# Kernel tuning notes

Measured on AMD Instinct MI355X. Metric: run time of the kernel, lower is better.

Reference implementation:

```python
import jax, jax.numpy as jnp
import numpy as np

B, S, D = 4, 4096, 1024


def setup_inputs() -> dict:
    key = jax.random.key(0)
    ks = jax.random.split(key, 4)
    scale = 1.0 / np.sqrt(D)
    x = jax.random.normal(ks[0], (B, S, D), dtype=jnp.float32)
    Wg = jax.random.normal(ks[1], (D, D), dtype=jnp.float32) * scale
    Wv = jax.random.normal(ks[2], (D, D), dtype=jnp.float32) * scale
    Wd = jax.random.normal(ks[3], (D, D), dtype=jnp.float32) * scale
    bg = jnp.zeros((D,), dtype=jnp.float32)
    bv = jnp.zeros((D,), dtype=jnp.float32)
    bd = jnp.ones((D,), dtype=jnp.float32)  # decay_bias_init = 1.0
    return {"x": x, "Wg": Wg, "bg": bg, "Wv": Wv, "bv": bv, "Wd": Wd, "bd": bd}


def _scan_causal(x_scan, a):
    # h_t = a_t * h_{t-1} + x_t, scanned over time; x_scan, a: [B,S,D]
    def step(h, inp):
        a_t, x_t = inp
        h = a_t * h + x_t
        return h, h

    h0 = jnp.zeros(x_scan.shape[::2], dtype=x_scan.dtype)  # [B,D]
    xs = (jnp.swapaxes(a, 0, 1), jnp.swapaxes(x_scan, 0, 1))  # [S,B,D]
    _, out = jax.lax.scan(step, h0, xs)
    return jnp.swapaxes(out, 0, 1)  # back to [B,S,D]


def reference(x, Wg, bg, Wv, bv, Wd, bd):
    # nn.Linear: y = x @ W.T + b
    g = jnp.einsum('bsd,ed->bse', x, Wg) + bg
    v = jnp.einsum('bsd,ed->bse', x, Wv) + bv
    d = jnp.einsum('bsd,ed->bse', x, Wd) + bd
    x_scan = jax.nn.sigmoid(g) * jnp.tanh(v)
    a = 0.001 + 0.998 * jax.nn.sigmoid(d)
    return _scan_causal(x_scan, a)
```

## Files before the change

### kernel.cpp

```cpp
#include <hip/hip_runtime.h>
#include <cstddef>
#include <cstdint>


typedef _Float16 f16;
typedef f16 f16x8 __attribute__((ext_vector_type(8)));
typedef float f32x4 __attribute__((ext_vector_type(4)));

#define S_LEN 4096
#define D_DIM 1024
#define B_DIM 4
#define M_TOT (B_DIM * S_LEN)
#define N_TOT (3 * D_DIM)
#define K_TOT D_DIM

#define CLEN 16
#define CPB (S_LEN / CLEN)
#define NCHUNK (B_DIM * CPB)

__device__ __forceinline__ void cvt8(const float* s, f16* d) {
  f32x4 a = *(const f32x4*)s;
  f32x4 b = *(const f32x4*)(s + 4);
  f16x8 o;
  o[0] = (f16)a[0]; o[1] = (f16)a[1]; o[2] = (f16)a[2]; o[3] = (f16)a[3];
  o[4] = (f16)b[0]; o[5] = (f16)b[1]; o[6] = (f16)b[2]; o[7] = (f16)b[3];
  *(f16x8*)d = o;
}

__global__ void cvt_all_kernel(const float* __restrict__ x, const float* __restrict__ w0,
                               const float* __restrict__ w1, const float* __restrict__ w2,
                               f16* __restrict__ Ah, f16* __restrict__ Bh) {
  int i = (blockIdx.x * 256 + threadIdx.x) * 8;
  if (i < M_TOT * K_TOT) {
    cvt8(x + i, Ah + i);
  } else {
    int w = i - M_TOT * K_TOT;
    int sel = w >> 20;
    int loc = w & 1048575;
    const float* s = (sel == 0) ? w0 : (sel == 1) ? w1 : w2;
    cvt8(s + loc, Bh + w);
  }
}

#define BM 128
#define BN 128
#define BK 32
#define CT_PITCH 136

__device__ __forceinline__ void gl_lds16(const void* g, void* l) {
  __builtin_amdgcn_global_load_lds((const __attribute__((address_space(1))) void*)g,
                                   (__attribute__((address_space(3))) void*)l, 16, 0, 0);
}

__global__ __launch_bounds__(256) void gemm_f16_kernel(const f16* __restrict__ A,
                                                       const f16* __restrict__ Bt,
                                                       f16* __restrict__ C) {
  __shared__ __attribute__((aligned(16))) char smem[BM * CT_PITCH * 2];
  f16* As = (f16*)smem;
  f16* Bs = As + 4096;
  const int tid = threadIdx.x;
  const int lane = tid & 63;
  const int wave = tid >> 6;
  const int m0 = blockIdx.y * BM;
  const int n0 = blockIdx.x * BN;

  const int srow = tid >> 2;
  const int scol = (tid & 3) * 8;
  const f16* aG0 = A + (size_t)(m0 + srow) * K_TOT + scol;
  const f16* aG1 = A + (size_t)(m0 + srow + 64) * K_TOT + scol;
  const f16* bG0 = Bt + (size_t)(n0 + srow) * K_TOT + scol;
  const f16* bG1 = Bt + (size_t)(n0 + srow + 64) * K_TOT + scol;
  f16* aL0 = As + tid * 8;
  f16* aL1 = As + 2048 + tid * 8;
  f16* bL0 = Bs + tid * 8;
  f16* bL1 = Bs + 2048 + tid * 8;

  const int wm = (wave >> 1) * 64;
  const int wn = (wave & 1) * 64;
  const int lm = lane & 15;
  const int kq = (lane >> 4) * 8;

  f32x4 acc[4][4] = {};

  for (int k0 = 0; k0 < K_TOT; k0 += BK) {
    gl_lds16(aG0 + k0, aL0);
    gl_lds16(aG1 + k0, aL1);
    gl_lds16(bG0 + k0, bL0);
    gl_lds16(bG1 + k0, bL1);
    __syncthreads();
    f16x8 af[4], bf[4];
#pragma unroll
    for (int i = 0; i < 4; ++i)
      af[i] = *(const f16x8*)&As[(wm + i * 16 + lm) * BK + kq];
#pragma unroll
    for (int j = 0; j < 4; ++j)
      bf[j] = *(const f16x8*)&Bs[(wn + j * 16 + lm) * BK + kq];
#pragma unroll
    for (int i = 0; i < 4; ++i)
#pragma unroll
      for (int j = 0; j < 4; ++j)
        acc[i][j] = __builtin_amdgcn_mfma_f32_16x16x32_f16(af[i], bf[j], acc[i][j], 0, 0, 0);
    __syncthreads();
  }

  f16* Ct = (f16*)smem;
  const int r0 = wm + (lane >> 4) * 4;
  const int c0 = wn + (lane & 15);
#pragma unroll
  for (int i = 0; i < 4; ++i)
#pragma unroll
    for (int j = 0; j < 4; ++j)
#pragma unroll
      for (int r = 0; r < 4; ++r)
        Ct[(r0 + i * 16 + r) * CT_PITCH + c0 + j * 16] = (f16)acc[i][j][r];
  __syncthreads();
#pragma unroll
  for (int p = 0; p < 8; ++p) {
    int row = p * 16 + (tid >> 4);
    int col = (tid & 15) * 8;
    *(f16x8*)(C + (size_t)(m0 + row) * N_TOT + n0 + col) =
        *(const f16x8*)&Ct[row * CT_PITCH + col];
  }
}

__global__ void scan1_kernel(const f16* __restrict__ G, const float* __restrict__ bg,
                             const float* __restrict__ bv, const float* __restrict__ bd,
                             f16* __restrict__ xsA, f16* __restrict__ aA,
                             float* __restrict__ P, float* __restrict__ H) {
  const int u = blockIdx.x * 256 + threadIdx.x;
  const int cg = u & 127;
  const int b = (u >> 7) & 3;
  const int ck = u >> 9;
  const int ch = cg * 8;
  float vbg[8], vbv[8], vbd[8];
  *(f32x4*)vbg = *(const f32x4*)(bg + ch); *(f32x4*)(vbg + 4) = *(const f32x4*)(bg + ch + 4);
  *(f32x4*)vbv = *(const f32x4*)(bv + ch); *(f32x4*)(vbv + 4) = *(const f32x4*)(bv + ch + 4);
  *(f32x4*)vbd = *(const f32x4*)(bd + ch); *(f32x4*)(vbd + 4) = *(const f32x4*)(bd + ch + 4);
  float h[8] = {}, p[8] = {1.f, 1.f, 1.f, 1.f, 1.f, 1.f, 1.f, 1.f};
  const int t0 = ck * CLEN;
#pragma unroll 2
  for (int t = t0; t < t0 + CLEN; ++t) {
    const size_t m = (size_t)b * S_LEN + t;
    const f16* gp = G + m * N_TOT + ch;
    f16x8 g8 = *(const f16x8*)gp;
    f16x8 v8 = *(const f16x8*)(gp + D_DIM);
    f16x8 d8 = *(const f16x8*)(gp + 2 * D_DIM);
    f16x8 xs8, a8;
#pragma unroll
    for (int j = 0; j < 8; ++j) {
      float gg = (float)g8[j] + vbg[j];
      float vv = (float)v8[j] + vbv[j];
      float dd = (float)d8[j] + vbd[j];
      float sg = 1.f / (1.f + __expf(-gg));
      float tv = 1.f - 2.f / (__expf(2.f * vv) + 1.f);
      float sd = 1.f / (1.f + __expf(-dd));
      f16 xh = (f16)(sg * tv);
      f16 ah = (f16)(0.001f + 0.998f * sd);
      float xsr = (float)xh, avr = (float)ah;
      h[j] = avr * h[j] + xsr;
      p[j] *= avr;
      xs8[j] = xh;
      a8[j] = ah;
    }
    *(f16x8*)(xsA + m * D_DIM + ch) = xs8;
    *(f16x8*)(aA + m * D_DIM + ch) = a8;
  }
  const int base = (b * CPB + ck) * D_DIM + ch;
  *(f32x4*)(P + base) = *(f32x4*)p;
  *(f32x4*)(P + base + 4) = *(f32x4*)(p + 4);
  *(f32x4*)(H + base) = *(f32x4*)h;
  *(f32x4*)(H + base + 4) = *(f32x4*)(h + 4);
}

__global__ void scan2_kernel(const float* __restrict__ P, const float* __restrict__ H,
                             float* __restrict__ carry) {
  const int idx = blockIdx.x * 256 + threadIdx.x;
  const int b = idx >> 10;
  const int d = idx & 1023;
  float h = 0.f;
  for (int c = 0; c < CPB; ++c) {
    int gs = b * CPB + c;
    carry[gs * D_DIM + d] = h;
    h = P[gs * D_DIM + d] * h + H[gs * D_DIM + d];
  }
}

__global__ void scan3_kernel(const f16* __restrict__ xsA, const f16* __restrict__ aA,
                             const float* __restrict__ carry, float* __restrict__ out) {
  const int u = blockIdx.x * 256 + threadIdx.x;
  const int cg = u & 127;
  const int b = (u >> 7) & 3;
  const int ck = u >> 9;
  const int ch = cg * 8;
  const int base = (b * CPB + ck) * D_DIM + ch;
  float h[8];
  *(f32x4*)h = *(const f32x4*)(carry + base);
  *(f32x4*)(h + 4) = *(const f32x4*)(carry + base + 4);
  const int t0 = ck * CLEN;
#pragma unroll 2
  for (int t = t0; t < t0 + CLEN; ++t) {
    const size_t m = (size_t)b * S_LEN + t;
    f16x8 xs8 = *(const f16x8*)(xsA + m * D_DIM + ch);
    f16x8 a8 = *(const f16x8*)(aA + m * D_DIM + ch);
#pragma unroll
    for (int j = 0; j < 8; ++j) h[j] = (float)a8[j] * h[j] + (float)xs8[j];
    float* op = out + m * D_DIM + ch;
    *(f32x4*)op = *(f32x4*)h;
    *(f32x4*)(op + 4) = *(f32x4*)(h + 4);
  }
}

extern "C" void kernel_launch(void* const* d_in, const int* in_sizes, int n_in,
                              void* d_out, int out_size, void* d_ws, size_t ws_size,
                              hipStream_t stream) {
  const float* x = (const float*)d_in[0];
  const float* Wg = (const float*)d_in[1];
  const float* bg = (const float*)d_in[2];
  const float* Wv = (const float*)d_in[3];
  const float* bv = (const float*)d_in[4];
  const float* Wd = (const float*)d_in[5];
  const float* bd = (const float*)d_in[6];
  float* out = (float*)d_out;

  char* ws = (char*)d_ws;
  f16* Ah = (f16*)(ws);
  float* P = (float*)(ws);
  float* H = (float*)(ws + 4194304);
  float* carry = (float*)(ws + 8388608);
  f16* Bh = (f16*)(ws + 33554432);
  f16* Gh = (f16*)(ws + 39845888);
  f16* xsA = (f16*)(ws + 140509184);
  f16* aA = (f16*)(ws + 174063616);

  cvt_all_kernel<<<9728, 256, 0, stream>>>(x, Wg, Wv, Wd, Ah, Bh);
  gemm_f16_kernel<<<dim3(N_TOT / BN, M_TOT / BM), 256, 0, stream>>>(Ah, Bh, Gh);
  scan1_kernel<<<512, 256, 0, stream>>>(Gh, bg, bv, bd, xsA, aA, P, H);
  scan2_kernel<<<16, 256, 0, stream>>>(P, H, carry);
  scan3_kernel<<<512, 256, 0, stream>>>(xsA, aA, carry, out);
}
```

Before: 338.2 us.

## Double GEMM K-tile to 64 and halve scan chunk length with transposed carries

The GEMM loads a 64-wide K slab per iteration as two 32-wide halves, which halves the number of barrier-separated iterations. The chunked scan uses 8-step chunks instead of 16, doubling thread count in the elementwise passes. It also stores per-chunk products and partial states transposed so the sequential carry pass can use vector loads. The trade-off is that the serial carry pass now has twice as many steps on very few threads.

```diff
diff --git a/kernel.cpp b/kernel.cpp
--- a/kernel.cpp
+++ b/kernel.cpp
@@ -14,7 +14,7 @@
 #define N_TOT (3 * D_DIM)
 #define K_TOT D_DIM
 
-#define CLEN 16
+#define CLEN 8
 #define CPB (S_LEN / CLEN)
 #define NCHUNK (B_DIM * CPB)
 
@@ -44,7 +44,6 @@
 
 #define BM 128
 #define BN 128
-#define BK 32
 #define CT_PITCH 136
 
 __device__ __forceinline__ void gl_lds16(const void* g, void* l) {
@@ -57,7 +56,7 @@
                                                        f16* __restrict__ C) {
   __shared__ __attribute__((aligned(16))) char smem[BM * CT_PITCH * 2];
   f16* As = (f16*)smem;
-  f16* Bs = As + 4096;
+  f16* Bs = As + 8192;
   const int tid = threadIdx.x;
   const int lane = tid & 63;
   const int wave = tid >> 6;
@@ -72,8 +71,12 @@
   const f16* bG1 = Bt + (size_t)(n0 + srow + 64) * K_TOT + scol;
   f16* aL0 = As + tid * 8;
   f16* aL1 = As + 2048 + tid * 8;
+  f16* aL2 = As + 4096 + tid * 8;
+  f16* aL3 = As + 6144 + tid * 8;
   f16* bL0 = Bs + tid * 8;
   f16* bL1 = Bs + 2048 + tid * 8;
+  f16* bL2 = Bs + 4096 + tid * 8;
+  f16* bL3 = Bs + 6144 + tid * 8;
 
   const int wm = (wave >> 1) * 64;
   const int wn = (wave & 1) * 64;
@@ -82,24 +85,33 @@
 
   f32x4 acc[4][4] = {};
 
-  for (int k0 = 0; k0 < K_TOT; k0 += BK) {
+  for (int k0 = 0; k0 < K_TOT; k0 += 64) {
     gl_lds16(aG0 + k0, aL0);
     gl_lds16(aG1 + k0, aL1);
+    gl_lds16(aG0 + k0 + 32, aL2);
+    gl_lds16(aG1 + k0 + 32, aL3);
     gl_lds16(bG0 + k0, bL0);
     gl_lds16(bG1 + k0, bL1);
+    gl_lds16(bG0 + k0 + 32, bL2);
+    gl_lds16(bG1 + k0 + 32, bL3);
     __syncthreads();
-    f16x8 af[4], bf[4];
-#pragma unroll
-    for (int i = 0; i < 4; ++i)
-      af[i] = *(const f16x8*)&As[(wm + i * 16 + lm) * BK + kq];
-#pragma unroll
-    for (int j = 0; j < 4; ++j)
-      bf[j] = *(const f16x8*)&Bs[(wn + j * 16 + lm) * BK + kq];
-#pragma unroll
-    for (int i = 0; i < 4; ++i)
+#pragma unroll
+    for (int h = 0; h < 2; ++h) {
+      const f16* as = As + h * 4096;
+      const f16* bs = Bs + h * 4096;
+      f16x8 af[4], bf[4];
+#pragma unroll
+      for (int i = 0; i < 4; ++i)
+        af[i] = *(const f16x8*)&as[(wm + i * 16 + lm) * 32 + kq];
 #pragma unroll
       for (int j = 0; j < 4; ++j)
-        acc[i][j] = __builtin_amdgcn_mfma_f32_16x16x32_f16(af[i], bf[j], acc[i][j], 0, 0, 0);
+        bf[j] = *(const f16x8*)&bs[(wn + j * 16 + lm) * 32 + kq];
+#pragma unroll
+      for (int i = 0; i < 4; ++i)
+#pragma unroll
+        for (int j = 0; j < 4; ++j)
+          acc[i][j] = __builtin_amdgcn_mfma_f32_16x16x32_f16(af[i], bf[j], acc[i][j], 0, 0, 0);
+    }
     __syncthreads();
   }
 
@@ -138,7 +150,7 @@
   *(f32x4*)vbd = *(const f32x4*)(bd + ch); *(f32x4*)(vbd + 4) = *(const f32x4*)(bd + ch + 4);
   float h[8] = {}, p[8] = {1.f, 1.f, 1.f, 1.f, 1.f, 1.f, 1.f, 1.f};
   const int t0 = ck * CLEN;
-#pragma unroll 2
+#pragma unroll
   for (int t = t0; t < t0 + CLEN; ++t) {
     const size_t m = (size_t)b * S_LEN + t;
     const f16* gp = G + m * N_TOT + ch;
@@ -165,23 +177,30 @@
     *(f16x8*)(xsA + m * D_DIM + ch) = xs8;
     *(f16x8*)(aA + m * D_DIM + ch) = a8;
   }
-  const int base = (b * CPB + ck) * D_DIM + ch;
-  *(f32x4*)(P + base) = *(f32x4*)p;
-  *(f32x4*)(P + base + 4) = *(f32x4*)(p + 4);
-  *(f32x4*)(H + base) = *(f32x4*)h;
-  *(f32x4*)(H + base + 4) = *(f32x4*)(h + 4);
+#pragma unroll
+  for (int j = 0; j < 8; ++j) {
+    const size_t tbase = (size_t)(b * D_DIM + ch + j) * CPB + ck;
+    P[tbase] = p[j];
+    H[tbase] = h[j];
+  }
 }
 
 __global__ void scan2_kernel(const float* __restrict__ P, const float* __restrict__ H,
                              float* __restrict__ carry) {
-  const int idx = blockIdx.x * 256 + threadIdx.x;
-  const int b = idx >> 10;
-  const int d = idx & 1023;
+  const int bd = blockIdx.x * 256 + threadIdx.x;
+  const int b = bd >> 10;
+  const int d = bd & 1023;
+  const float* Pp = P + (size_t)bd * CPB;
+  const float* Hp = H + (size_t)bd * CPB;
   float h = 0.f;
-  for (int c = 0; c < CPB; ++c) {
-    int gs = b * CPB + c;
-    carry[gs * D_DIM + d] = h;
-    h = P[gs * D_DIM + d] * h + H[gs * D_DIM + d];
+  for (int c = 0; c < CPB; c += 4) {
+    f32x4 p4 = *(const f32x4*)(Pp + c);
+    f32x4 h4 = *(const f32x4*)(Hp + c);
+    float* cp = carry + (size_t)(b * CPB + c) * D_DIM + d;
+    cp[0] = h;          h = p4[0] * h + h4[0];
+    cp[D_DIM] = h;      h = p4[1] * h + h4[1];
+    cp[2 * D_DIM] = h;  h = p4[2] * h + h4[2];
+    cp[3 * D_DIM] = h;  h = p4[3] * h + h4[3];
   }
 }
 
@@ -192,12 +211,12 @@
   const int b = (u >> 7) & 3;
   const int ck = u >> 9;
   const int ch = cg * 8;
-  const int base = (b * CPB + ck) * D_DIM + ch;
+  const size_t base = (size_t)(b * CPB + ck) * D_DIM + ch;
   float h[8];
   *(f32x4*)h = *(const f32x4*)(carry + base);
   *(f32x4*)(h + 4) = *(const f32x4*)(carry + base + 4);
   const int t0 = ck * CLEN;
-#pragma unroll 2
+#pragma unroll
   for (int t = t0; t < t0 + CLEN; ++t) {
     const size_t m = (size_t)b * S_LEN + t;
     f16x8 xs8 = *(const f16x8*)(xsA + m * D_DIM + ch);
@@ -225,8 +244,8 @@
   char* ws = (char*)d_ws;
   f16* Ah = (f16*)(ws);
   float* P = (float*)(ws);
-  float* H = (float*)(ws + 4194304);
-  float* carry = (float*)(ws + 8388608);
+  float* H = (float*)(ws + 8388608);
+  float* carry = (float*)(ws + 16777216);
   f16* Bh = (f16*)(ws + 33554432);
   f16* Gh = (f16*)(ws + 39845888);
   f16* xsA = (f16*)(ws + 140509184);
@@ -234,7 +253,7 @@
 
   cvt_all_kernel<<<9728, 256, 0, stream>>>(x, Wg, Wv, Wd, Ah, Bh);
   gemm_f16_kernel<<<dim3(N_TOT / BN, M_TOT / BM), 256, 0, stream>>>(Ah, Bh, Gh);
-  scan1_kernel<<<512, 256, 0, stream>>>(Gh, bg, bv, bd, xsA, aA, P, H);
+  scan1_kernel<<<1024, 256, 0, stream>>>(Gh, bg, bv, bd, xsA, aA, P, H);
   scan2_kernel<<<16, 256, 0, stream>>>(P, H, carry);
-  scan3_kernel<<<512, 256, 0, stream>>>(xsA, aA, carry, out);
-}
+  scan3_kernel<<<1024, 256, 0, stream>>>(xsA, aA, carry, out);
+}
```

After: 378.4 us. +11.9%, slower.

## Fuse three scan kernels into one cooperative kernel with grid syncs

Applied to the files above, without the earlier changes.

Replaces the three-pass chunked scan with one cooperative kernel. Each thread keeps its chunk's gated inputs and decays in registers across two grid-wide barriers instead of writing them to and re-reading them from global memory. This removes the f16 xs/a round trip through HBM and two kernel launches. In exchange it needs co-residency of 1024 blocks, raises register pressure, and runs the serial carry pass on only 4096 threads between the barriers; if the cooperative launch fails it falls back to the old three kernels.

```diff
diff --git a/kernel.cpp b/kernel.cpp
--- a/kernel.cpp
+++ b/kernel.cpp
@@ -1,9 +1,13 @@
 #include <hip/hip_runtime.h>
+#include <hip/hip_cooperative_groups.h>
 #include <cstddef>
 #include <cstdint>
 
+namespace cg = cooperative_groups;
+
 
 typedef _Float16 f16;
+typedef f16 f16x4 __attribute__((ext_vector_type(4)));
 typedef f16 f16x8 __attribute__((ext_vector_type(8)));
 typedef float f32x4 __attribute__((ext_vector_type(4)));
 
@@ -123,15 +127,92 @@
   }
 }
 
+__device__ __forceinline__ void act(float g, float v, float d, f16& xh, f16& ah) {
+  float sg = 1.f / (1.f + __expf(-g));
+  float tv = 1.f - 2.f / (__expf(2.f * v) + 1.f);
+  float sd = 1.f / (1.f + __expf(-d));
+  xh = (f16)(sg * tv);
+  ah = (f16)(0.001f + 0.998f * sd);
+}
+
+__global__ __launch_bounds__(256, 4) void fused_scan_kernel(
+    const f16* __restrict__ G, const float* __restrict__ bg,
+    const float* __restrict__ bv, const float* __restrict__ bd,
+    float* __restrict__ P, float* __restrict__ H, float* __restrict__ carry,
+    float* __restrict__ out) {
+  cg::grid_group grid = cg::this_grid();
+  const int u = blockIdx.x * 256 + threadIdx.x;
+  const int cgi = u & 255;
+  const int b = (u >> 8) & 3;
+  const int ck = u >> 10;
+  const int ch = cgi * 4;
+  const int gs = b * CPB + ck;
+  const int t0 = ck * CLEN;
+
+  const f32x4 vbg = *(const f32x4*)(bg + ch);
+  const f32x4 vbv = *(const f32x4*)(bv + ch);
+  const f32x4 vbd = *(const f32x4*)(bd + ch);
+
+  f16x4 xsr[CLEN], ar[CLEN];
+  f32x4 h = {0.f, 0.f, 0.f, 0.f};
+  f32x4 p = {1.f, 1.f, 1.f, 1.f};
+#pragma unroll
+  for (int i = 0; i < CLEN; ++i) {
+    const size_t m = (size_t)b * S_LEN + (t0 + i);
+    const f16* gp = G + m * N_TOT + ch;
+    f16x4 g4 = *(const f16x4*)gp;
+    f16x4 v4 = *(const f16x4*)(gp + D_DIM);
+    f16x4 d4 = *(const f16x4*)(gp + 2 * D_DIM);
+#pragma unroll
+    for (int j = 0; j < 4; ++j) {
+      f16 xh, ah;
+      act((float)g4[j] + vbg[j], (float)v4[j] + vbv[j], (float)d4[j] + vbd[j], xh, ah);
+      xsr[i][j] = xh;
+      ar[i][j] = ah;
+      float xf = (float)xh, af = (float)ah;
+      h[j] = af * h[j] + xf;
+      p[j] *= af;
+    }
+  }
+  *(f32x4*)(P + (size_t)gs * D_DIM + ch) = p;
+  *(f32x4*)(H + (size_t)gs * D_DIM + ch) = h;
+
+  grid.sync();
+
+  if (u < B_DIM * D_DIM) {
+    const int b2 = u >> 10;
+    const int d2 = u & 1023;
+    float hh = 0.f;
+#pragma unroll 4
+    for (int c = 0; c < CPB; ++c) {
+      const size_t idx = (size_t)(b2 * CPB + c) * D_DIM + d2;
+      carry[idx] = hh;
+      hh = P[idx] * hh + H[idx];
+    }
+  }
+
+  grid.sync();
+
+  f32x4 hc = *(const f32x4*)(carry + (size_t)gs * D_DIM + ch);
+#pragma unroll
+  for (int i = 0; i < CLEN; ++i) {
+    const size_t m = (size_t)b * S_LEN + (t0 + i);
+#pragma unroll
+    for (int j = 0; j < 4; ++j)
+      hc[j] = (float)ar[i][j] * hc[j] + (float)xsr[i][j];
+    *(f32x4*)(out + m * D_DIM + ch) = hc;
+  }
+}
+
 __global__ void scan1_kernel(const f16* __restrict__ G, const float* __restrict__ bg,
                              const float* __restrict__ bv, const float* __restrict__ bd,
                              f16* __restrict__ xsA, f16* __restrict__ aA,
                              float* __restrict__ P, float* __restrict__ H) {
   const int u = blockIdx.x * 256 + threadIdx.x;
-  const int cg = u & 127;
+  const int cgi = u & 127;
   const int b = (u >> 7) & 3;
   const int ck = u >> 9;
-  const int ch = cg * 8;
+  const int ch = cgi * 8;
   float vbg[8], vbv[8], vbd[8];
   *(f32x4*)vbg = *(const f32x4*)(bg + ch); *(f32x4*)(vbg + 4) = *(const f32x4*)(bg + ch + 4);
   *(f32x4*)vbv = *(const f32x4*)(bv + ch); *(f32x4*)(vbv + 4) = *(const f32x4*)(bv + ch + 4);
@@ -148,16 +229,10 @@
     f16x8 xs8, a8;
 #pragma unroll
     for (int j = 0; j < 8; ++j) {
-      float gg = (float)g8[j] + vbg[j];
-      float vv = (float)v8[j] + vbv[j];
-      float dd = (float)d8[j] + vbd[j];
-      float sg = 1.f / (1.f + __expf(-gg));
-      float tv = 1.f - 2.f / (__expf(2.f * vv) + 1.f);
-      float sd = 1.f / (1.f + __expf(-dd));
-      f16 xh = (f16)(sg * tv);
-      f16 ah = (f16)(0.001f + 0.998f * sd);
-      float xsr = (float)xh, avr = (float)ah;
-      h[j] = avr * h[j] + xsr;
+      f16 xh, ah;
+      act((float)g8[j] + vbg[j], (float)v8[j] + vbv[j], (float)d8[j] + vbd[j], xh, ah);
+      float xsrv = (float)xh, avr = (float)ah;
+      h[j] = avr * h[j] + xsrv;
       p[j] *= avr;
       xs8[j] = xh;
       a8[j] = ah;
@@ -179,19 +254,19 @@
   const int d = idx & 1023;
   float h = 0.f;
   for (int c = 0; c < CPB; ++c) {
-    int gs = b * CPB + c;
-    carry[gs * D_DIM + d] = h;
-    h = P[gs * D_DIM + d] * h + H[gs * D_DIM + d];
+    int gsb = b * CPB + c;
+    carry[gsb * D_DIM + d] = h;
+    h = P[gsb * D_DIM + d] * h + H[gsb * D_DIM + d];
   }
 }
 
 __global__ void scan3_kernel(const f16* __restrict__ xsA, const f16* __restrict__ aA,
                              const float* __restrict__ carry, float* __restrict__ out) {
   const int u = blockIdx.x * 256 + threadIdx.x;
-  const int cg = u & 127;
+  const int cgi = u & 127;
   const int b = (u >> 7) & 3;
   const int ck = u >> 9;
-  const int ch = cg * 8;
+  const int ch = cgi * 8;
   const int base = (b * CPB + ck) * D_DIM + ch;
   float h[8];
   *(f32x4*)h = *(const f32x4*)(carry + base);
@@ -234,7 +309,14 @@
 
   cvt_all_kernel<<<9728, 256, 0, stream>>>(x, Wg, Wv, Wd, Ah, Bh);
   gemm_f16_kernel<<<dim3(N_TOT / BN, M_TOT / BM), 256, 0, stream>>>(Ah, Bh, Gh);
-  scan1_kernel<<<512, 256, 0, stream>>>(Gh, bg, bv, bd, xsA, aA, P, H);
-  scan2_kernel<<<16, 256, 0, stream>>>(P, H, carry);
-  scan3_kernel<<<512, 256, 0, stream>>>(xsA, aA, carry, out);
-}
+
+  void* args[] = {(void*)&Gh, (void*)&bg, (void*)&bv, (void*)&bd,
+                  (void*)&P, (void*)&H, (void*)&carry, (void*)&out};
+  hipError_t rc = hipLaunchCooperativeKernel((const void*)fused_scan_kernel,
+                                             dim3(1024), dim3(256), args, 0, stream);
+  if (rc != hipSuccess) {
+    scan1_kernel<<<512, 256, 0, stream>>>(Gh, bg, bv, bd, xsA, aA, P, H);
+    scan2_kernel<<<16, 256, 0, stream>>>(P, H, carry);
+    scan3_kernel<<<512, 256, 0, stream>>>(xsA, aA, carry, out);
+  }
+}
```

Result: slower. 619.1 us (+83.0%).

## Fuse gate activations and chunk-local scan into GEMM epilogue with interleaved weights

Applied to the files above, without the earlier changes.

Interleaves the three weight matrices row-wise so each 96-column GEMM tile holds matching g/v/d columns for 32 channels. The activations, the 16-step chunk scan (P,H) and the xs/a stores then run in the GEMM epilogue, which removes the scan1 kernel and the round trip of the fp16 G intermediate through global memory. The cost is a narrower N tile (3 MFMA columns per wave, half the threads loading B on the second row group), which lowers per-block MFMA density and adds a serial epilogue per block.

```diff
diff --git a/kernel.cpp b/kernel.cpp
--- a/kernel.cpp
+++ b/kernel.cpp
@@ -35,141 +35,134 @@
     cvt8(x + i, Ah + i);
   } else {
     int w = i - M_TOT * K_TOT;
-    int sel = w >> 20;
-    int loc = w & 1048575;
-    const float* s = (sel == 0) ? w0 : (sel == 1) ? w1 : w2;
-    cvt8(s + loc, Bh + w);
+    int row = w >> 10;
+    int col = w & 1023;
+    int srow = row / 3;
+    int mat = row - srow * 3;
+    const float* s = (mat == 0) ? w0 : (mat == 1) ? w1 : w2;
+    cvt8(s + srow * 1024 + col, Bh + w);
   }
 }
 
 #define BM 128
-#define BN 128
+#define BN 96
 #define BK 32
-#define CT_PITCH 136
+#define RAWP 100
+#define XSP 32
 
 __device__ __forceinline__ void gl_lds16(const void* g, void* l) {
   __builtin_amdgcn_global_load_lds((const __attribute__((address_space(1))) void*)g,
                                    (__attribute__((address_space(3))) void*)l, 16, 0, 0);
 }
 
-__global__ __launch_bounds__(256) void gemm_f16_kernel(const f16* __restrict__ A,
-                                                       const f16* __restrict__ Bt,
-                                                       f16* __restrict__ C) {
-  __shared__ __attribute__((aligned(16))) char smem[BM * CT_PITCH * 2];
-  f16* As = (f16*)smem;
-  f16* Bs = As + 4096;
+__device__ __forceinline__ void act(float g, float v, float d, f16& xh, f16& ah) {
+  float sg = 1.f / (1.f + __expf(-g));
+  float tv = 1.f - 2.f / (__expf(2.f * v) + 1.f);
+  float sd = 1.f / (1.f + __expf(-d));
+  xh = (f16)(sg * tv);
+  ah = (f16)(0.001f + 0.998f * sd);
+}
+
+__global__ __launch_bounds__(256) void gemm_fused_kernel(
+    const f16* __restrict__ A, const f16* __restrict__ Bt,
+    const float* __restrict__ bg, const float* __restrict__ bv,
+    const float* __restrict__ bd,
+    f16* __restrict__ xsA, f16* __restrict__ aA,
+    float* __restrict__ P, float* __restrict__ H) {
+  __shared__ __attribute__((aligned(16))) f16 smem[20992];
+  f16* As = smem;
+  f16* Bs = smem + 4096;
   const int tid = threadIdx.x;
   const int lane = tid & 63;
   const int wave = tid >> 6;
   const int m0 = blockIdx.y * BM;
-  const int n0 = blockIdx.x * BN;
+  const int bn0 = blockIdx.x * BN;
 
   const int srow = tid >> 2;
   const int scol = (tid & 3) * 8;
   const f16* aG0 = A + (size_t)(m0 + srow) * K_TOT + scol;
   const f16* aG1 = A + (size_t)(m0 + srow + 64) * K_TOT + scol;
-  const f16* bG0 = Bt + (size_t)(n0 + srow) * K_TOT + scol;
-  const f16* bG1 = Bt + (size_t)(n0 + srow + 64) * K_TOT + scol;
+  const f16* bG0 = Bt + (size_t)(bn0 + srow) * K_TOT + scol;
+  const f16* bG1 = Bt + (size_t)(bn0 + 64 + (tid >> 2)) * K_TOT + scol;
   f16* aL0 = As + tid * 8;
   f16* aL1 = As + 2048 + tid * 8;
   f16* bL0 = Bs + tid * 8;
   f16* bL1 = Bs + 2048 + tid * 8;
 
   const int wm = (wave >> 1) * 64;
-  const int wn = (wave & 1) * 64;
+  const int wn = (wave & 1) * 48;
   const int lm = lane & 15;
   const int kq = (lane >> 4) * 8;
 
-  f32x4 acc[4][4] = {};
+  f32x4 acc[4][3] = {};
 
   for (int k0 = 0; k0 < K_TOT; k0 += BK) {
     gl_lds16(aG0 + k0, aL0);
     gl_lds16(aG1 + k0, aL1);
     gl_lds16(bG0 + k0, bL0);
-    gl_lds16(bG1 + k0, bL1);
+    if (tid < 128) gl_lds16(bG1 + k0, bL1);
     __syncthreads();
-    f16x8 af[4], bf[4];
+    f16x8 af[4], bf[3];
 #pragma unroll
     for (int i = 0; i < 4; ++i)
       af[i] = *(const f16x8*)&As[(wm + i * 16 + lm) * BK + kq];
 #pragma unroll
-    for (int j = 0; j < 4; ++j)
+    for (int j = 0; j < 3; ++j)
       bf[j] = *(const f16x8*)&Bs[(wn + j * 16 + lm) * BK + kq];
 #pragma unroll
     for (int i = 0; i < 4; ++i)
 #pragma unroll
-      for (int j = 0; j < 4; ++j)
+      for (int j = 0; j < 3; ++j)
         acc[i][j] = __builtin_amdgcn_mfma_f32_16x16x32_f16(af[i], bf[j], acc[i][j], 0, 0, 0);
     __syncthreads();
   }
 
-  f16* Ct = (f16*)smem;
+  f16* Raw = smem;
   const int r0 = wm + (lane >> 4) * 4;
   const int c0 = wn + (lane & 15);
 #pragma unroll
   for (int i = 0; i < 4; ++i)
 #pragma unroll
-    for (int j = 0; j < 4; ++j)
+    for (int j = 0; j < 3; ++j)
 #pragma unroll
       for (int r = 0; r < 4; ++r)
-        Ct[(r0 + i * 16 + r) * CT_PITCH + c0 + j * 16] = (f16)acc[i][j][r];
+        Raw[(r0 + i * 16 + r) * RAWP + c0 + j * 16] = (f16)acc[i][j][r];
   __syncthreads();
-#pragma unroll
-  for (int p = 0; p < 8; ++p) {
-    int row = p * 16 + (tid >> 4);
-    int col = (tid & 15) * 8;
-    *(f16x8*)(C + (size_t)(m0 + row) * N_TOT + n0 + col) =
-        *(const f16x8*)&Ct[row * CT_PITCH + col];
-  }
-}
-
-__global__ void scan1_kernel(const f16* __restrict__ G, const float* __restrict__ bg,
-                             const float* __restrict__ bv, const float* __restrict__ bd,
-                             f16* __restrict__ xsA, f16* __restrict__ aA,
-                             float* __restrict__ P, float* __restrict__ H) {
-  const int u = blockIdx.x * 256 + threadIdx.x;
-  const int cg = u & 127;
-  const int b = (u >> 7) & 3;
-  const int ck = u >> 9;
-  const int ch = cg * 8;
-  float vbg[8], vbv[8], vbd[8];
-  *(f32x4*)vbg = *(const f32x4*)(bg + ch); *(f32x4*)(vbg + 4) = *(const f32x4*)(bg + ch + 4);
-  *(f32x4*)vbv = *(const f32x4*)(bv + ch); *(f32x4*)(vbv + 4) = *(const f32x4*)(bv + ch + 4);
-  *(f32x4*)vbd = *(const f32x4*)(bd + ch); *(f32x4*)(vbd + 4) = *(const f32x4*)(bd + ch + 4);
-  float h[8] = {}, p[8] = {1.f, 1.f, 1.f, 1.f, 1.f, 1.f, 1.f, 1.f};
-  const int t0 = ck * CLEN;
-#pragma unroll 2
-  for (int t = t0; t < t0 + CLEN; ++t) {
-    const size_t m = (size_t)b * S_LEN + t;
-    const f16* gp = G + m * N_TOT + ch;
-    f16x8 g8 = *(const f16x8*)gp;
-    f16x8 v8 = *(const f16x8*)(gp + D_DIM);
-    f16x8 d8 = *(const f16x8*)(gp + 2 * D_DIM);
-    f16x8 xs8, a8;
-#pragma unroll
-    for (int j = 0; j < 8; ++j) {
-      float gg = (float)g8[j] + vbg[j];
-      float vv = (float)v8[j] + vbv[j];
-      float dd = (float)d8[j] + vbd[j];
-      float sg = 1.f / (1.f + __expf(-gg));
-      float tv = 1.f - 2.f / (__expf(2.f * vv) + 1.f);
-      float sd = 1.f / (1.f + __expf(-dd));
-      f16 xh = (f16)(sg * tv);
-      f16 ah = (f16)(0.001f + 0.998f * sd);
-      float xsr = (float)xh, avr = (float)ah;
-      h[j] = avr * h[j] + xsr;
-      p[j] *= avr;
-      xs8[j] = xh;
-      a8[j] = ah;
+
+  f16* xsL = smem + 12800;
+  f16* aL = smem + 16896;
+  {
+    const int d = tid & 31;
+    const int c = tid >> 5;
+    const int gd = (blockIdx.x << 5) + d;
+    const float Bg = bg[gd], Bv = bv[gd], Bd_ = bd[gd];
+    float p = 1.f, h = 0.f;
+#pragma unroll
+    for (int i = 0; i < CLEN; ++i) {
+      const int r = c * CLEN + i;
+      const f16* t3 = &Raw[r * RAWP + 3 * d];
+      f16 xh, ah;
+      act((float)t3[0] + Bg, (float)t3[1] + Bv, (float)t3[2] + Bd_, xh, ah);
+      xsL[r * XSP + d] = xh;
+      aL[r * XSP + d] = ah;
+      float xf = (float)xh, af_ = (float)ah;
+      h = af_ * h + xf;
+      p *= af_;
     }
-    *(f16x8*)(xsA + m * D_DIM + ch) = xs8;
-    *(f16x8*)(aA + m * D_DIM + ch) = a8;
-  }
-  const int base = (b * CPB + ck) * D_DIM + ch;
-  *(f32x4*)(P + base) = *(f32x4*)p;
-  *(f32x4*)(P + base + 4) = *(f32x4*)(p + 4);
-  *(f32x4*)(H + base) = *(f32x4*)h;
-  *(f32x4*)(H + base + 4) = *(f32x4*)(h + 4);
+    const int gs = (m0 >> 4) + c;
+    P[(size_t)gs * D_DIM + gd] = p;
+    H[(size_t)gs * D_DIM + gd] = h;
+  }
+  __syncthreads();
+
+#pragma unroll
+  for (int rr = 0; rr < 2; ++rr) {
+    const int row = rr * 64 + (tid >> 2);
+    const int col = (tid & 3) * 8;
+    const size_t gi = (size_t)(m0 + row) * D_DIM + (blockIdx.x << 5) + col;
+    *(f16x8*)(xsA + gi) = *(const f16x8*)&xsL[row * XSP + col];
+    *(f16x8*)(aA + gi) = *(const f16x8*)&aL[row * XSP + col];
+  }
 }
 
 __global__ void scan2_kernel(const float* __restrict__ P, const float* __restrict__ H,
@@ -224,17 +217,16 @@
 
   char* ws = (char*)d_ws;
   f16* Ah = (f16*)(ws);
-  float* P = (float*)(ws);
-  float* H = (float*)(ws + 4194304);
-  float* carry = (float*)(ws + 8388608);
   f16* Bh = (f16*)(ws + 33554432);
-  f16* Gh = (f16*)(ws + 39845888);
-  f16* xsA = (f16*)(ws + 140509184);
-  f16* aA = (f16*)(ws + 174063616);
+  f16* xsA = (f16*)(ws + 39845888);
+  f16* aA = (f16*)(ws + 73400320);
+  float* P = (float*)(ws + 106954752);
+  float* H = (float*)(ws + 111149056);
+  float* carry = (float*)(ws + 115343360);
 
   cvt_all_kernel<<<9728, 256, 0, stream>>>(x, Wg, Wv, Wd, Ah, Bh);
-  gemm_f16_kernel<<<dim3(N_TOT / BN, M_TOT / BM), 256, 0, stream>>>(Ah, Bh, Gh);
-  scan1_kernel<<<512, 256, 0, stream>>>(Gh, bg, bv, bd, xsA, aA, P, H);
+  gemm_fused_kernel<<<dim3(N_TOT / BN, M_TOT / BM), 256, 0, stream>>>(
+      Ah, Bh, bg, bv, bd, xsA, aA, P, H);
   scan2_kernel<<<16, 256, 0, stream>>>(P, H, carry);
   scan3_kernel<<<512, 256, 0, stream>>>(xsA, aA, carry, out);
 }
```

Result: faster. 327.5 us (-3.2%).
